# Optimization experiments

Hardware: AMD Instinct MI355X
Metric: run time of the kernel (lower is better)

Reference implementation:

```python
import jax, jax.numpy as jnp
import numpy as np

H = 4096        # hidden_size
NH = 32         # num query heads
NKV = 8         # num kv heads
HD = H // NH    # head_dim = 128
T_PREV = 16383  # cached tokens; new token makes T = 16384
BASE = 10000.0


def _rope(x, pos):
    # x: [heads, head_dim]; interleaved even/odd RoPE at a single position
    d = x.shape[-1]
    inv_freq = 1.0 / (BASE ** (jnp.arange(0, d, 2, dtype=jnp.float32) / d))
    f = pos * inv_freq                      # [d/2]
    c, s = jnp.cos(f), jnp.sin(f)
    xe, xo = x[..., 0::2], x[..., 1::2]
    out = jnp.stack([xe * c - xo * s, xe * s + xo * c], axis=-1)
    return out.reshape(x.shape)


def setup_inputs() -> dict:
    key = jax.random.key(0)
    ks = jax.random.split(key, 7)
    w = 0.02  # weight scale for numerical stability
    return {
        "hidden": jax.random.normal(ks[0], (H,), jnp.float32),
        "k_cache": jax.random.normal(ks[1], (T_PREV, NKV, HD), jnp.float32),
        "v_cache": jax.random.normal(ks[2], (T_PREV, NKV, HD), jnp.float32),
        "Wq": jax.random.normal(ks[3], (H, H), jnp.float32) * w,
        "Wk": jax.random.normal(ks[4], (NKV * HD, H), jnp.float32) * w,
        "Wv": jax.random.normal(ks[5], (NKV * HD, H), jnp.float32) * w,
        "Wo": jax.random.normal(ks[6], (H, H), jnp.float32) * w,
        "position_id": T_PREV,
    }


def reference(hidden, k_cache, v_cache, Wq, Wk, Wv, Wo, position_id):
    pos = jnp.float32(position_id)
    # projections (nn.Linear: y = W @ x), single token
    q = (Wq @ hidden).reshape(NH, HD)
    k = (Wk @ hidden).reshape(NKV, HD)
    v = (Wv @ hidden).reshape(NKV, HD)
    # inline RoPE on new q and k
    q = _rope(q, pos)
    k = _rope(k, pos)
    # contiguous KV including the new token
    k_all = jnp.concatenate([k_cache, k[None]], axis=0)   # [T, NKV, HD]
    v_all = jnp.concatenate([v_cache, v[None]], axis=0)
    # GQA: repeat KV heads to match query heads
    rep = NH // NKV
    k_all = jnp.repeat(k_all, rep, axis=1)                 # [T, NH, HD]
    v_all = jnp.repeat(v_all, rep, axis=1)
    # single-query attention
    scores = jnp.einsum('hd,thd->ht', q, k_all) / jnp.sqrt(jnp.float32(HD))
    attn = jax.nn.softmax(scores, axis=-1)                 # [NH, T]
    ctx = jnp.einsum('ht,thd->hd', attn, v_all)            # [NH, HD]
    # combine heads + output projection
    return Wo @ ctx.reshape(H)
```

## Files before the change

kernel.cpp:

```cpp
#include <hip/hip_runtime.h>
#include <math.h>

#define NH 32
#define NKV 8
#define HD 128
#define HDIM 4096
#define KVDIM 1024
#define TPREV 16383
#define NCHUNK 128
#define CHUNK 128

#define OFF_Q 0
#define OFF_K 4096
#define OFF_V 5120
#define OFF_PART 6144
#define PART_STRIDE 130
#define OFF_CTX (OFF_PART + NH * NCHUNK * PART_STRIDE)

__device__ __forceinline__ float wave_reduce_sum(float v) {
#pragma unroll
  for (int m = 32; m >= 1; m >>= 1) v += __shfl_xor(v, m, 64);
  return v;
}
__device__ __forceinline__ float wave_reduce_max(float v) {
#pragma unroll
  for (int m = 32; m >= 1; m >>= 1) v = fmaxf(v, __shfl_xor(v, m, 64));
  return v;
}

__global__ __launch_bounds__(256) void qkv_rope_kernel(
    const float* __restrict__ Wq, const float* __restrict__ Wk,
    const float* __restrict__ Wv, const float* __restrict__ hidden,
    const int* __restrict__ pos_p, float* __restrict__ ws) {
  int r = blockIdx.x * 4 + (threadIdx.x >> 6);
  int lane = threadIdx.x & 63;
  const float* W;
  int wr;
  if (r < HDIM) {
    W = Wq; wr = r;
  } else if (r < HDIM + KVDIM) {
    W = Wk; wr = r - HDIM;
  } else {
    W = Wv; wr = r - HDIM - KVDIM;
  }
  const float4* w4 = (const float4*)(W + (size_t)wr * HDIM);
  const float4* h4 = (const float4*)hidden;
  float s = 0.f;
#pragma unroll
  for (int i = 0; i < 16; ++i) {
    float4 a = w4[lane + 64 * i];
    float4 b = h4[lane + 64 * i];
    s += a.x * b.x + a.y * b.y + a.z * b.z + a.w * b.w;
  }
  s = wave_reduce_sum(s);
  __shared__ float rs[4];
  if (lane == 0) rs[threadIdx.x >> 6] = s;
  __syncthreads();
  if (threadIdx.x < 2) {
    int r0 = blockIdx.x * 4 + (int)threadIdx.x * 2;
    float S0 = rs[threadIdx.x * 2], S1 = rs[threadIdx.x * 2 + 1];
    if (r0 < HDIM + KVDIM) {
      int j = (r0 & (HD - 1)) >> 1;
      double f = (double)(*pos_p) * pow(10000.0, -(double)j / 64.0);
      float c = (float)cos(f), sn = (float)sin(f);
      ws[r0] = S0 * c - S1 * sn;
      ws[r0 + 1] = S0 * sn + S1 * c;
    } else {
      ws[r0] = S0;
      ws[r0 + 1] = S1;
    }
  }
}

__global__ __launch_bounds__(256) void attn_chunk_kernel(
    const float* __restrict__ k_cache, const float* __restrict__ v_cache,
    float* __restrict__ ws) {
  int g = blockIdx.x >> 7;
  int c = blockIdx.x & 127;
  int t0 = c * CHUNK;
  int tid = threadIdx.x;

  __shared__ float qs[4 * HD];
  __shared__ float sc[CHUNK * 5];
  __shared__ float vacc[8][4][HD];
  __shared__ float wredm[4][4], wredl[4][4];
  __shared__ float mh[4], lh[4];

  for (int i = tid; i < 4 * HD; i += 256) qs[i] = ws[OFF_Q + g * 4 * HD + i];
  __syncthreads();

  const float rscale = 0.08838834764831845f;
  int grp = tid >> 5, lane = tid & 31;

  for (int it = grp; it < CHUNK; it += 8) {
    int t = t0 + it;
    if (t < TPREV) {
      float4 kv = ((const float4*)(k_cache + (size_t)t * KVDIM + g * HD))[lane];
      float4 q0 = ((const float4*)(qs + 0 * HD))[lane];
      float4 q1 = ((const float4*)(qs + 1 * HD))[lane];
      float4 q2 = ((const float4*)(qs + 2 * HD))[lane];
      float4 q3 = ((const float4*)(qs + 3 * HD))[lane];
      float s0 = kv.x * q0.x + kv.y * q0.y + kv.z * q0.z + kv.w * q0.w;
      float s1 = kv.x * q1.x + kv.y * q1.y + kv.z * q1.z + kv.w * q1.w;
      float s2 = kv.x * q2.x + kv.y * q2.y + kv.z * q2.z + kv.w * q2.w;
      float s3 = kv.x * q3.x + kv.y * q3.y + kv.z * q3.z + kv.w * q3.w;
#pragma unroll
      for (int m = 16; m >= 1; m >>= 1) {
        s0 += __shfl_xor(s0, m, 64);
        s1 += __shfl_xor(s1, m, 64);
        s2 += __shfl_xor(s2, m, 64);
        s3 += __shfl_xor(s3, m, 64);
      }
      if (lane == 0) {
        sc[it * 5 + 0] = s0 * rscale;
        sc[it * 5 + 1] = s1 * rscale;
        sc[it * 5 + 2] = s2 * rscale;
        sc[it * 5 + 3] = s3 * rscale;
      }
    } else if (lane == 0) {
      sc[it * 5 + 0] = -1e30f;
      sc[it * 5 + 1] = -1e30f;
      sc[it * 5 + 2] = -1e30f;
      sc[it * 5 + 3] = -1e30f;
    }
  }
  __syncthreads();

  float m0 = -1e30f, m1 = -1e30f, m2 = -1e30f, m3 = -1e30f;
  if (tid < CHUNK) {
    m0 = sc[tid * 5 + 0]; m1 = sc[tid * 5 + 1];
    m2 = sc[tid * 5 + 2]; m3 = sc[tid * 5 + 3];
  }
  m0 = wave_reduce_max(m0); m1 = wave_reduce_max(m1);
  m2 = wave_reduce_max(m2); m3 = wave_reduce_max(m3);
  if ((tid & 63) == 0) {
    int w = tid >> 6;
    wredm[w][0] = m0; wredm[w][1] = m1; wredm[w][2] = m2; wredm[w][3] = m3;
  }
  __syncthreads();
  if (tid < 4)
    mh[tid] = fmaxf(fmaxf(wredm[0][tid], wredm[1][tid]),
                    fmaxf(wredm[2][tid], wredm[3][tid]));
  __syncthreads();

  float M0 = mh[0], M1 = mh[1], M2 = mh[2], M3 = mh[3];
  float e0 = 0.f, e1 = 0.f, e2 = 0.f, e3 = 0.f;
  if (tid < CHUNK) {
    e0 = expf(sc[tid * 5 + 0] - M0);
    e1 = expf(sc[tid * 5 + 1] - M1);
    e2 = expf(sc[tid * 5 + 2] - M2);
    e3 = expf(sc[tid * 5 + 3] - M3);
    sc[tid * 5 + 0] = e0;
    sc[tid * 5 + 1] = e1;
    sc[tid * 5 + 2] = e2;
    sc[tid * 5 + 3] = e3;
  }
  float l0 = wave_reduce_sum(e0);
  float l1 = wave_reduce_sum(e1);
  float l2 = wave_reduce_sum(e2);
  float l3 = wave_reduce_sum(e3);
  if ((tid & 63) == 0) {
    int w = tid >> 6;
    wredl[w][0] = l0; wredl[w][1] = l1; wredl[w][2] = l2; wredl[w][3] = l3;
  }
  __syncthreads();
  if (tid < 4)
    lh[tid] = wredl[0][tid] + wredl[1][tid] + wredl[2][tid] + wredl[3][tid];
  __syncthreads();

  float4 a0 = {0, 0, 0, 0}, a1 = {0, 0, 0, 0}, a2 = {0, 0, 0, 0},
         a3 = {0, 0, 0, 0};
  for (int it = grp; it < CHUNK; it += 8) {
    int t = t0 + it;
    if (t < TPREV) {
      float4 v = ((const float4*)(v_cache + (size_t)t * KVDIM + g * HD))[lane];
      float p0 = sc[it * 5 + 0], p1 = sc[it * 5 + 1];
      float p2 = sc[it * 5 + 2], p3 = sc[it * 5 + 3];
      a0.x = fmaf(p0, v.x, a0.x); a0.y = fmaf(p0, v.y, a0.y);
      a0.z = fmaf(p0, v.z, a0.z); a0.w = fmaf(p0, v.w, a0.w);
      a1.x = fmaf(p1, v.x, a1.x); a1.y = fmaf(p1, v.y, a1.y);
      a1.z = fmaf(p1, v.z, a1.z); a1.w = fmaf(p1, v.w, a1.w);
      a2.x = fmaf(p2, v.x, a2.x); a2.y = fmaf(p2, v.y, a2.y);
      a2.z = fmaf(p2, v.z, a2.z); a2.w = fmaf(p2, v.w, a2.w);
      a3.x = fmaf(p3, v.x, a3.x); a3.y = fmaf(p3, v.y, a3.y);
      a3.z = fmaf(p3, v.z, a3.z); a3.w = fmaf(p3, v.w, a3.w);
    }
  }
  ((float4*)&vacc[grp][0][0])[lane] = a0;
  ((float4*)&vacc[grp][1][0])[lane] = a1;
  ((float4*)&vacc[grp][2][0])[lane] = a2;
  ((float4*)&vacc[grp][3][0])[lane] = a3;
  __syncthreads();

  float* part = ws + OFF_PART;
#pragma unroll
  for (int rep = 0; rep < 2; ++rep) {
    int p = tid + rep * 256;
    int h = p >> 7, d = p & 127;
    float s = 0.f;
#pragma unroll
    for (int g2 = 0; g2 < 8; ++g2) s += vacc[g2][h][d];
    part[(size_t)((g * 4 + h) * NCHUNK + c) * PART_STRIDE + d] = s;
  }
  if (tid < 4) {
    part[(size_t)((g * 4 + tid) * NCHUNK + c) * PART_STRIDE + 128] = mh[tid];
    part[(size_t)((g * 4 + tid) * NCHUNK + c) * PART_STRIDE + 129] = lh[tid];
  }
}

__global__ __launch_bounds__(256) void combine_kernel(float* __restrict__ ws) {
  int h = blockIdx.x;
  int g = h >> 2;
  int tid = threadIdx.x;
  const float rscale = 0.08838834764831845f;
  const float* ph = ws + OFF_PART + (size_t)h * NCHUNK * PART_STRIDE;

  __shared__ float red[HD];
  __shared__ float wexp[NCHUNK];
  __shared__ float wm[4], wl[4];
  __shared__ float acc2[HD];

  if (tid < HD) red[tid] = ws[OFF_Q + h * HD + tid] * ws[OFF_K + g * HD + tid];
  __syncthreads();
#pragma unroll
  for (int s2 = 64; s2 >= 1; s2 >>= 1) {
    if (tid < s2 && tid + s2 < HD) red[tid] += red[tid + s2];
    __syncthreads();
  }
  float snew = red[0] * rscale;

  float mloc = -1e30f;
  if (tid < NCHUNK) {
    mloc = ph[tid * PART_STRIDE + 128];
    wexp[tid] = mloc;
  }
  float mm = wave_reduce_max(fmaxf(mloc, snew));
  if ((tid & 63) == 0) wm[tid >> 6] = mm;
  __syncthreads();
  float M = fmaxf(fmaxf(wm[0], wm[1]), fmaxf(wm[2], wm[3]));

  float lpart = 0.f;
  if (tid < NCHUNK) {
    float w = expf(wexp[tid] - M);
    lpart = ph[tid * PART_STRIDE + 129] * w;
    wexp[tid] = w;
  }
  float lsum = wave_reduce_sum(lpart);
  if ((tid & 63) == 0) wl[tid >> 6] = lsum;
  __syncthreads();
  float en = expf(snew - M);
  float L = wl[0] + wl[1] + wl[2] + wl[3] + en;

  int half = tid >> 7, d = tid & 127;
  float acc = 0.f;
  int cbeg = half * 64;
#pragma unroll 4
  for (int c2 = cbeg; c2 < cbeg + 64; ++c2)
    acc = fmaf(ph[(size_t)c2 * PART_STRIDE + d], wexp[c2], acc);
  if (half == 0) acc2[d] = acc;
  __syncthreads();
  if (half == 1) acc2[d] += acc;
  __syncthreads();
  if (tid < HD)
    ws[OFF_CTX + h * HD + tid] =
        (acc2[tid] + en * ws[OFF_V + g * HD + tid]) / L;
}

__global__ __launch_bounds__(256) void out_matvec_kernel(
    const float* __restrict__ Wo, const float* __restrict__ ws,
    float* __restrict__ out) {
  int r = blockIdx.x * 4 + (threadIdx.x >> 6);
  int lane = threadIdx.x & 63;
  const float4* w4 = (const float4*)(Wo + (size_t)r * HDIM);
  const float4* x4 = (const float4*)(ws + OFF_CTX);
  float s = 0.f;
#pragma unroll
  for (int i = 0; i < 16; ++i) {
    float4 a = w4[lane + 64 * i];
    float4 b = x4[lane + 64 * i];
    s += a.x * b.x + a.y * b.y + a.z * b.z + a.w * b.w;
  }
  s = wave_reduce_sum(s);
  if (lane == 0) out[r] = s;
}

extern "C" void kernel_launch(void* const* d_in, const int* in_sizes, int n_in,
                              void* d_out, int out_size, void* d_ws,
                              size_t ws_size, hipStream_t stream) {
  const float* hidden = (const float*)d_in[0];
  const float* k_cache = (const float*)d_in[1];
  const float* v_cache = (const float*)d_in[2];
  const float* Wq = (const float*)d_in[3];
  const float* Wk = (const float*)d_in[4];
  const float* Wv = (const float*)d_in[5];
  const float* Wo = (const float*)d_in[6];
  const int* pos = (const int*)d_in[7];
  float* out = (float*)d_out;
  float* ws = (float*)d_ws;

  qkv_rope_kernel<<<(HDIM + 2 * KVDIM) / 4, 256, 0, stream>>>(Wq, Wk, Wv,
                                                              hidden, pos, ws);
  attn_chunk_kernel<<<NKV * NCHUNK, 256, 0, stream>>>(k_cache, v_cache, ws);
  combine_kernel<<<NH, 256, 0, stream>>>(ws);
  out_matvec_kernel<<<HDIM / 4, 256, 0, stream>>>(Wo, ws, out);
}
```

Measured before the change: 290.7 us.

## Restructure attention chunks to thread-per-token scoring and batch global loads

Doubles the attention chunk size, which halves the number of partial results the combine kernel has to merge. In the QK phase each thread now computes a full dot product for one token, which removes the shared-memory score round trip and the per-token shuffle reductions. The V accumulation and the QKV/output matvecs now issue batches of float4 loads before doing the arithmetic, to raise memory-level parallelism. The trade-offs are that each thread reads K rows with a 4 KB stride between neighbouring threads, which coalesces poorly, and that register pressure goes up; a 2-blocks-per-SM occupancy hint is added to manage it.

```diff
diff --git a/kernel.cpp b/kernel.cpp
--- a/kernel.cpp
+++ b/kernel.cpp
@@ -7,8 +7,8 @@
 #define HDIM 4096
 #define KVDIM 1024
 #define TPREV 16383
-#define NCHUNK 128
-#define CHUNK 128
+#define NCHUNK 64
+#define CHUNK 256
 
 #define OFF_Q 0
 #define OFF_K 4096
@@ -26,6 +26,9 @@
 #pragma unroll
   for (int m = 32; m >= 1; m >>= 1) v = fmaxf(v, __shfl_xor(v, m, 64));
   return v;
+}
+__device__ __forceinline__ float dot4(float4 a, float4 b) {
+  return a.x * b.x + a.y * b.y + a.z * b.z + a.w * b.w;
 }
 
 __global__ __launch_bounds__(256) void qkv_rope_kernel(
@@ -47,10 +50,14 @@
   const float4* h4 = (const float4*)hidden;
   float s = 0.f;
 #pragma unroll
-  for (int i = 0; i < 16; ++i) {
-    float4 a = w4[lane + 64 * i];
-    float4 b = h4[lane + 64 * i];
-    s += a.x * b.x + a.y * b.y + a.z * b.z + a.w * b.w;
+  for (int base = 0; base < 16; base += 8) {
+    float4 a[8], b[8];
+#pragma unroll
+    for (int j = 0; j < 8; ++j) a[j] = w4[lane + 64 * (base + j)];
+#pragma unroll
+    for (int j = 0; j < 8; ++j) b[j] = h4[lane + 64 * (base + j)];
+#pragma unroll
+    for (int j = 0; j < 8; ++j) s += dot4(a[j], b[j]);
   }
   s = wave_reduce_sum(s);
   __shared__ float rs[4];
@@ -72,11 +79,11 @@
   }
 }
 
-__global__ __launch_bounds__(256) void attn_chunk_kernel(
+__global__ __launch_bounds__(256, 2) void attn_chunk_kernel(
     const float* __restrict__ k_cache, const float* __restrict__ v_cache,
     float* __restrict__ ws) {
-  int g = blockIdx.x >> 7;
-  int c = blockIdx.x & 127;
+  int g = blockIdx.x >> 6;
+  int c = blockIdx.x & 63;
   int t0 = c * CHUNK;
   int tid = threadIdx.x;
 
@@ -90,49 +97,32 @@
   __syncthreads();
 
   const float rscale = 0.08838834764831845f;
-  int grp = tid >> 5, lane = tid & 31;
-
-  for (int it = grp; it < CHUNK; it += 8) {
-    int t = t0 + it;
-    if (t < TPREV) {
-      float4 kv = ((const float4*)(k_cache + (size_t)t * KVDIM + g * HD))[lane];
-      float4 q0 = ((const float4*)(qs + 0 * HD))[lane];
-      float4 q1 = ((const float4*)(qs + 1 * HD))[lane];
-      float4 q2 = ((const float4*)(qs + 2 * HD))[lane];
-      float4 q3 = ((const float4*)(qs + 3 * HD))[lane];
-      float s0 = kv.x * q0.x + kv.y * q0.y + kv.z * q0.z + kv.w * q0.w;
-      float s1 = kv.x * q1.x + kv.y * q1.y + kv.z * q1.z + kv.w * q1.w;
-      float s2 = kv.x * q2.x + kv.y * q2.y + kv.z * q2.z + kv.w * q2.w;
-      float s3 = kv.x * q3.x + kv.y * q3.y + kv.z * q3.z + kv.w * q3.w;
-#pragma unroll
-      for (int m = 16; m >= 1; m >>= 1) {
-        s0 += __shfl_xor(s0, m, 64);
-        s1 += __shfl_xor(s1, m, 64);
-        s2 += __shfl_xor(s2, m, 64);
-        s3 += __shfl_xor(s3, m, 64);
+
+  int tok = t0 + tid;
+  bool valid = tok < TPREV;
+  float s0 = -1e30f, s1 = -1e30f, s2 = -1e30f, s3 = -1e30f;
+  if (valid) {
+    const float4* kp = (const float4*)(k_cache + (size_t)tok * KVDIM + g * HD);
+    const float4* q4 = (const float4*)qs;
+    s0 = 0.f; s1 = 0.f; s2 = 0.f; s3 = 0.f;
+#pragma unroll
+    for (int base = 0; base < 32; base += 8) {
+      float4 kk[8];
+#pragma unroll
+      for (int j = 0; j < 8; ++j) kk[j] = kp[base + j];
+#pragma unroll
+      for (int j = 0; j < 8; ++j) {
+        s0 += dot4(kk[j], q4[0 * 32 + base + j]);
+        s1 += dot4(kk[j], q4[1 * 32 + base + j]);
+        s2 += dot4(kk[j], q4[2 * 32 + base + j]);
+        s3 += dot4(kk[j], q4[3 * 32 + base + j]);
       }
-      if (lane == 0) {
-        sc[it * 5 + 0] = s0 * rscale;
-        sc[it * 5 + 1] = s1 * rscale;
-        sc[it * 5 + 2] = s2 * rscale;
-        sc[it * 5 + 3] = s3 * rscale;
-      }
-    } else if (lane == 0) {
-      sc[it * 5 + 0] = -1e30f;
-      sc[it * 5 + 1] = -1e30f;
-      sc[it * 5 + 2] = -1e30f;
-      sc[it * 5 + 3] = -1e30f;
-    }
-  }
-  __syncthreads();
-
-  float m0 = -1e30f, m1 = -1e30f, m2 = -1e30f, m3 = -1e30f;
-  if (tid < CHUNK) {
-    m0 = sc[tid * 5 + 0]; m1 = sc[tid * 5 + 1];
-    m2 = sc[tid * 5 + 2]; m3 = sc[tid * 5 + 3];
-  }
-  m0 = wave_reduce_max(m0); m1 = wave_reduce_max(m1);
-  m2 = wave_reduce_max(m2); m3 = wave_reduce_max(m3);
+    }
+    s0 *= rscale; s1 *= rscale; s2 *= rscale; s3 *= rscale;
+  }
+
+  float m0 = wave_reduce_max(s0), m1 = wave_reduce_max(s1);
+  float m2 = wave_reduce_max(s2), m3 = wave_reduce_max(s3);
   if ((tid & 63) == 0) {
     int w = tid >> 6;
     wredm[w][0] = m0; wredm[w][1] = m1; wredm[w][2] = m2; wredm[w][3] = m3;
@@ -143,22 +133,14 @@
                     fmaxf(wredm[2][tid], wredm[3][tid]));
   __syncthreads();
 
-  float M0 = mh[0], M1 = mh[1], M2 = mh[2], M3 = mh[3];
-  float e0 = 0.f, e1 = 0.f, e2 = 0.f, e3 = 0.f;
-  if (tid < CHUNK) {
-    e0 = expf(sc[tid * 5 + 0] - M0);
-    e1 = expf(sc[tid * 5 + 1] - M1);
-    e2 = expf(sc[tid * 5 + 2] - M2);
-    e3 = expf(sc[tid * 5 + 3] - M3);
-    sc[tid * 5 + 0] = e0;
-    sc[tid * 5 + 1] = e1;
-    sc[tid * 5 + 2] = e2;
-    sc[tid * 5 + 3] = e3;
-  }
-  float l0 = wave_reduce_sum(e0);
-  float l1 = wave_reduce_sum(e1);
-  float l2 = wave_reduce_sum(e2);
-  float l3 = wave_reduce_sum(e3);
+  float e0 = expf(s0 - mh[0]), e1 = expf(s1 - mh[1]);
+  float e2 = expf(s2 - mh[2]), e3 = expf(s3 - mh[3]);
+  sc[tid * 5 + 0] = e0;
+  sc[tid * 5 + 1] = e1;
+  sc[tid * 5 + 2] = e2;
+  sc[tid * 5 + 3] = e3;
+  float l0 = wave_reduce_sum(e0), l1 = wave_reduce_sum(e1);
+  float l2 = wave_reduce_sum(e2), l3 = wave_reduce_sum(e3);
   if ((tid & 63) == 0) {
     int w = tid >> 6;
     wredl[w][0] = l0; wredl[w][1] = l1; wredl[w][2] = l2; wredl[w][3] = l3;
@@ -168,22 +150,34 @@
     lh[tid] = wredl[0][tid] + wredl[1][tid] + wredl[2][tid] + wredl[3][tid];
   __syncthreads();
 
+  int grp = tid >> 5, lane = tid & 31;
   float4 a0 = {0, 0, 0, 0}, a1 = {0, 0, 0, 0}, a2 = {0, 0, 0, 0},
          a3 = {0, 0, 0, 0};
-  for (int it = grp; it < CHUNK; it += 8) {
-    int t = t0 + it;
-    if (t < TPREV) {
-      float4 v = ((const float4*)(v_cache + (size_t)t * KVDIM + g * HD))[lane];
+  const float4 z4 = {0, 0, 0, 0};
+#pragma unroll
+  for (int base = 0; base < 32; base += 4) {
+    float4 vv[4];
+#pragma unroll
+    for (int j = 0; j < 4; ++j) {
+      int it = grp + 8 * (base + j);
+      int t = t0 + it;
+      vv[j] = (t < TPREV)
+                  ? ((const float4*)(v_cache + (size_t)t * KVDIM + g * HD))[lane]
+                  : z4;
+    }
+#pragma unroll
+    for (int j = 0; j < 4; ++j) {
+      int it = grp + 8 * (base + j);
       float p0 = sc[it * 5 + 0], p1 = sc[it * 5 + 1];
       float p2 = sc[it * 5 + 2], p3 = sc[it * 5 + 3];
-      a0.x = fmaf(p0, v.x, a0.x); a0.y = fmaf(p0, v.y, a0.y);
-      a0.z = fmaf(p0, v.z, a0.z); a0.w = fmaf(p0, v.w, a0.w);
-      a1.x = fmaf(p1, v.x, a1.x); a1.y = fmaf(p1, v.y, a1.y);
-      a1.z = fmaf(p1, v.z, a1.z); a1.w = fmaf(p1, v.w, a1.w);
-      a2.x = fmaf(p2, v.x, a2.x); a2.y = fmaf(p2, v.y, a2.y);
-      a2.z = fmaf(p2, v.z, a2.z); a2.w = fmaf(p2, v.w, a2.w);
-      a3.x = fmaf(p3, v.x, a3.x); a3.y = fmaf(p3, v.y, a3.y);
-      a3.z = fmaf(p3, v.z, a3.z); a3.w = fmaf(p3, v.w, a3.w);
+      a0.x = fmaf(p0, vv[j].x, a0.x); a0.y = fmaf(p0, vv[j].y, a0.y);
+      a0.z = fmaf(p0, vv[j].z, a0.z); a0.w = fmaf(p0, vv[j].w, a0.w);
+      a1.x = fmaf(p1, vv[j].x, a1.x); a1.y = fmaf(p1, vv[j].y, a1.y);
+      a1.z = fmaf(p1, vv[j].z, a1.z); a1.w = fmaf(p1, vv[j].w, a1.w);
+      a2.x = fmaf(p2, vv[j].x, a2.x); a2.y = fmaf(p2, vv[j].y, a2.y);
+      a2.z = fmaf(p2, vv[j].z, a2.z); a2.w = fmaf(p2, vv[j].w, a2.w);
+      a3.x = fmaf(p3, vv[j].x, a3.x); a3.y = fmaf(p3, vv[j].y, a3.y);
+      a3.z = fmaf(p3, vv[j].z, a3.z); a3.w = fmaf(p3, vv[j].w, a3.w);
     }
   }
   ((float4*)&vacc[grp][0][0])[lane] = a0;
@@ -217,7 +211,7 @@
 
   __shared__ float red[HD];
   __shared__ float wexp[NCHUNK];
-  __shared__ float wm[4], wl[4];
+  __shared__ float Msh, Lsh;
   __shared__ float acc2[HD];
 
   if (tid < HD) red[tid] = ws[OFF_Q + h * HD + tid] * ws[OFF_K + g * HD + tid];
@@ -229,33 +223,25 @@
   }
   float snew = red[0] * rscale;
 
-  float mloc = -1e30f;
-  if (tid < NCHUNK) {
-    mloc = ph[tid * PART_STRIDE + 128];
-    wexp[tid] = mloc;
-  }
-  float mm = wave_reduce_max(fmaxf(mloc, snew));
-  if ((tid & 63) == 0) wm[tid >> 6] = mm;
-  __syncthreads();
-  float M = fmaxf(fmaxf(wm[0], wm[1]), fmaxf(wm[2], wm[3]));
-
-  float lpart = 0.f;
-  if (tid < NCHUNK) {
-    float w = expf(wexp[tid] - M);
-    lpart = ph[tid * PART_STRIDE + 129] * w;
+  if (tid < 64) {
+    float m = ph[tid * PART_STRIDE + 128];
+    float M = wave_reduce_max(fmaxf(m, snew));
+    float w = expf(m - M);
+    float lp = ph[tid * PART_STRIDE + 129] * w;
+    float L = wave_reduce_sum(lp);
     wexp[tid] = w;
-  }
-  float lsum = wave_reduce_sum(lpart);
-  if ((tid & 63) == 0) wl[tid >> 6] = lsum;
-  __syncthreads();
+    if (tid == 0) { Msh = M; Lsh = L; }
+  }
+  __syncthreads();
+  float M = Msh;
   float en = expf(snew - M);
-  float L = wl[0] + wl[1] + wl[2] + wl[3] + en;
+  float L = Lsh + en;
 
   int half = tid >> 7, d = tid & 127;
   float acc = 0.f;
-  int cbeg = half * 64;
-#pragma unroll 4
-  for (int c2 = cbeg; c2 < cbeg + 64; ++c2)
+  int cbeg = half * 32;
+#pragma unroll 8
+  for (int c2 = cbeg; c2 < cbeg + 32; ++c2)
     acc = fmaf(ph[(size_t)c2 * PART_STRIDE + d], wexp[c2], acc);
   if (half == 0) acc2[d] = acc;
   __syncthreads();
@@ -275,10 +261,14 @@
   const float4* x4 = (const float4*)(ws + OFF_CTX);
   float s = 0.f;
 #pragma unroll
-  for (int i = 0; i < 16; ++i) {
-    float4 a = w4[lane + 64 * i];
-    float4 b = x4[lane + 64 * i];
-    s += a.x * b.x + a.y * b.y + a.z * b.z + a.w * b.w;
+  for (int base = 0; base < 16; base += 8) {
+    float4 a[8], b[8];
+#pragma unroll
+    for (int j = 0; j < 8; ++j) a[j] = w4[lane + 64 * (base + j)];
+#pragma unroll
+    for (int j = 0; j < 8; ++j) b[j] = x4[lane + 64 * (base + j)];
+#pragma unroll
+    for (int j = 0; j < 8; ++j) s += dot4(a[j], b[j]);
   }
   s = wave_reduce_sum(s);
   if (lane == 0) out[r] = s;
```

New measurement: 286.9 us. No clear change (-1.3%).
